# Kernel optimization log

Measured on AMD Instinct MI355X. Metric: run time of the kernel, lower is better.

The kernel has to match this reference:

```python
import jax, jax.numpy as jnp
import numpy as np

B, N, E, L, H, D = 16, 128, 2048, 4, 8, 64


def setup_inputs() -> dict:
    key = jax.random.key(0)
    k1, k2, k3, k4, k5 = jax.random.split(key, 5)
    edge_feat = jax.random.normal(k1, (B, E, D), dtype=jnp.float32)
    # index E (== num edges) is the zero-feature padding slot
    path_idx = jax.random.randint(k2, (B, N, N, L), 0, E + 1).astype(jnp.int32)
    dist = jax.random.randint(k3, (B, N, N), 0, L + 1).astype(jnp.int32)
    node_counts = jax.random.randint(k4, (B,), N // 2, N + 1).astype(jnp.int32)
    emb_table = jax.random.normal(k5, (L * H, D), dtype=jnp.float32)
    return {"edge_feat": edge_feat, "path_idx": path_idx, "dist": dist,
            "node_counts": node_counts, "emb_table": emb_table}


def reference(edge_feat, path_idx, dist, node_counts, emb_table):
    b, e, d = edge_feat.shape
    n = path_idx.shape[1]
    l = path_idx.shape[-1]
    h = emb_table.shape[0] // l
    # append zero row so padding index e gathers zeros (torch: cat zeros row)
    edata = jnp.concatenate([edge_feat, jnp.zeros((b, 1, d), edge_feat.dtype)], axis=1)
    # ragged per-graph path gather, batched: (b, n, n, l, d)
    path_data = jax.vmap(lambda ef, p: ef[p])(edata, path_idx)
    # embedding_idx = arange(h*l).reshape(l, h) -> table rows reshape to (l, h, d)
    emb = emb_table.reshape(l, h, d)
    # torch: einsum('xyld,dlh->xyh') with emb permuted (d,l,h); equivalent here
    enc = jnp.einsum('bxyld,lhd->bxyh', path_data, emb)
    dist_c = jnp.clip(dist, 1, l).astype(enc.dtype)  # clamp(min=1, max=path_len)
    enc = enc / dist_c[..., None]
    ar = jnp.arange(n)
    valid = (ar[None, :, None] < node_counts[:, None, None]) & \
            (ar[None, None, :] < node_counts[:, None, None])  # (b, n, n)
    neg_inf = jnp.asarray(-jnp.inf, enc.dtype)
    return jnp.where(valid[..., None], enc, neg_inf)
```

## Files before the change

kernel.cpp:

```cpp
#include <hip/hip_runtime.h>
#include <hip/hip_bf16.h>
#include <math.h>

#define BB 16
#define NN 128
#define EE 2048
#define LL 4
#define HH 8
#define DD 64
#define LH 32

#define NEG_SENTINEL (-1.0e30f)

typedef __attribute__((ext_vector_type(8))) short bf16x8;
typedef __attribute__((ext_vector_type(4))) float f32x4;

__device__ inline short f2bf(float f) {
    __hip_bfloat16 h = __float2bfloat16(f);
    return *(short*)&h;
}

__device__ inline bf16x8 pack_bf8(float4 a, float4 b) {
    bf16x8 r;
    r[0] = f2bf(a.x); r[1] = f2bf(a.y); r[2] = f2bf(a.z); r[3] = f2bf(a.w);
    r[4] = f2bf(b.x); r[5] = f2bf(b.y); r[6] = f2bf(b.z); r[7] = f2bf(b.w);
    return r;
}

__global__ __launch_bounds__(256) void precompute_proj_mfma(
    const float* __restrict__ edge_feat,
    const float* __restrict__ emb,
    __hip_bfloat16* __restrict__ proj)
{
    const int lane = threadIdx.x & 63;
    const int wave = threadIdx.x >> 6;
    const int tile = blockIdx.x * 4 + wave;
    const int row0 = tile * 16;
    const int m    = lane & 15;
    const int quad = lane >> 4;

    const float* arow = edge_feat + (size_t)(row0 + m) * DD + quad * 8;
    const float4 a00 = ((const float4*)arow)[0];
    const float4 a01 = ((const float4*)arow)[1];
    const float4 a10 = ((const float4*)(arow + 32))[0];
    const float4 a11 = ((const float4*)(arow + 32))[1];

    const float* br0 = emb + (size_t)m * DD + quad * 8;
    const float* br1 = emb + (size_t)(16 + m) * DD + quad * 8;
    const float4 b000 = ((const float4*)br0)[0];
    const float4 b001 = ((const float4*)br0)[1];
    const float4 b010 = ((const float4*)(br0 + 32))[0];
    const float4 b011 = ((const float4*)(br0 + 32))[1];
    const float4 b100 = ((const float4*)br1)[0];
    const float4 b101 = ((const float4*)br1)[1];
    const float4 b110 = ((const float4*)(br1 + 32))[0];
    const float4 b111 = ((const float4*)(br1 + 32))[1];

    const bf16x8 aK0  = pack_bf8(a00, a01);
    const bf16x8 aK1  = pack_bf8(a10, a11);
    const bf16x8 b0K0 = pack_bf8(b000, b001);
    const bf16x8 b0K1 = pack_bf8(b010, b011);
    const bf16x8 b1K0 = pack_bf8(b100, b101);
    const bf16x8 b1K1 = pack_bf8(b110, b111);

    f32x4 acc0 = {0.f, 0.f, 0.f, 0.f};
    f32x4 acc1 = {0.f, 0.f, 0.f, 0.f};
    acc0 = __builtin_amdgcn_mfma_f32_16x16x32_bf16(aK0, b0K0, acc0, 0, 0, 0);
    acc0 = __builtin_amdgcn_mfma_f32_16x16x32_bf16(aK1, b0K1, acc0, 0, 0, 0);
    acc1 = __builtin_amdgcn_mfma_f32_16x16x32_bf16(aK0, b1K0, acc1, 0, 0, 0);
    acc1 = __builtin_amdgcn_mfma_f32_16x16x32_bf16(aK1, b1K1, acc1, 0, 0, 0);

#pragma unroll
    for (int r = 0; r < 4; ++r) {
        const int row = row0 + quad * 4 + r;
        proj[row * LH + m]      = __float2bfloat16(acc0[r]);
        proj[row * LH + 16 + m] = __float2bfloat16(acc1[r]);
    }
}

__global__ __launch_bounds__(256) void path_gather(
    const int* __restrict__ path_idx,
    const int* __restrict__ dist,
    const int* __restrict__ node_counts,
    const __hip_bfloat16* __restrict__ proj,
    __hip_bfloat16* __restrict__ out)
{
    const int pos = blockIdx.x * blockDim.x + threadIdx.x;
    const int y   = pos & (NN - 1);
    const int x   = (pos >> 7) & (NN - 1);
    const int b   = pos >> 14;

    const int4 idx4 = ((const int4*)path_idx)[pos];
    const int  dv   = dist[pos];
    const int  nc   = node_counts[b];

    const uint4* pb = (const uint4*)(proj + (size_t)b * EE * LH);

    const int idx[4] = {idx4.x, idx4.y, idx4.z, idx4.w};
    float s[HH];
#pragma unroll
    for (int h = 0; h < HH; ++h) s[h] = 0.f;

#pragma unroll
    for (int l = 0; l < LL; ++l) {
        const int  ii    = idx[l];
        const bool live  = (ii < EE);
        uint4 v = pb[min(ii, EE - 1) * 4 + l];
        if (!live) { v.x = 0u; v.y = 0u; v.z = 0u; v.w = 0u; }
        const unsigned u[4] = {v.x, v.y, v.z, v.w};
#pragma unroll
        for (int p = 0; p < 4; ++p) {
            float flo = __uint_as_float(u[p] << 16);
            float fhi = __uint_as_float(u[p] & 0xFFFF0000u);
            s[2 * p + 0] += flo;
            s[2 * p + 1] += fhi;
        }
    }

    const int   dc = dv < 1 ? 1 : (dv > LL ? LL : dv);
    const float rd = 1.0f / (float)dc;
    const bool valid = (x < nc) && (y < nc);

    uint4 ov;
    unsigned short* po = (unsigned short*)&ov;
#pragma unroll
    for (int h = 0; h < HH; ++h) {
        const float r = valid ? s[h] * rd : NEG_SENTINEL;
        __hip_bfloat16 bh = __float2bfloat16(r);
        po[h] = *(unsigned short*)&bh;
    }
    ((uint4*)out)[pos] = ov;
}

extern "C" void kernel_launch(void* const* d_in, const int* in_sizes, int n_in,
                              void* d_out, int out_size, void* d_ws, size_t ws_size,
                              hipStream_t stream) {
    const float* edge_feat   = (const float*)d_in[0];
    const int*   path_idx    = (const int*)d_in[1];
    const int*   dist        = (const int*)d_in[2];
    const int*   node_counts = (const int*)d_in[3];
    const float* emb_table   = (const float*)d_in[4];
    __hip_bfloat16* out = (__hip_bfloat16*)d_out;

    __hip_bfloat16* proj = (__hip_bfloat16*)d_ws;

    precompute_proj_mfma<<<512, 256, 0, stream>>>(edge_feat, emb_table, proj);

    path_gather<<<1024, 256, 0, stream>>>(path_idx, dist, node_counts, proj, out);
}
```

Before: 78.04 us.

## Fuse projection and gather into one cooperative kernel with grid sync

Merges the MFMA edge-projection kernel and the path-gather kernel into one cooperative launch. A grid-wide barrier separates the two phases, so the second kernel launch and the gap between launches go away. If the cooperative launch fails, it falls back to the original two launches. The cost is the grid-sync overhead. The 1024-block grid must also stay co-resident, and half the blocks sit idle during the projection phase.

```diff
diff --git a/kernel.cpp b/kernel.cpp
--- a/kernel.cpp
+++ b/kernel.cpp
@@ -1,6 +1,9 @@
 #include <hip/hip_runtime.h>
 #include <hip/hip_bf16.h>
+#include <hip/hip_cooperative_groups.h>
 #include <math.h>
+
+namespace cg = cooperative_groups;
 
 #define BB 16
 #define NN 128
@@ -27,14 +30,12 @@
     return r;
 }
 
-__global__ __launch_bounds__(256) void precompute_proj_mfma(
+__device__ __forceinline__ void proj_tile_body(
     const float* __restrict__ edge_feat,
     const float* __restrict__ emb,
-    __hip_bfloat16* __restrict__ proj)
-{
-    const int lane = threadIdx.x & 63;
-    const int wave = threadIdx.x >> 6;
-    const int tile = blockIdx.x * 4 + wave;
+    __hip_bfloat16* __restrict__ proj,
+    int tile, int lane)
+{
     const int row0 = tile * 16;
     const int m    = lane & 15;
     const int quad = lane >> 4;
@@ -78,6 +79,93 @@
     }
 }
 
+__device__ __forceinline__ void gather_body(
+    const int* __restrict__ path_idx,
+    const int* __restrict__ dist,
+    const int* __restrict__ node_counts,
+    const __hip_bfloat16* __restrict__ proj,
+    __hip_bfloat16* __restrict__ out,
+    int pos)
+{
+    const int y = pos & (NN - 1);
+    const int x = (pos >> 7) & (NN - 1);
+    const int b = pos >> 14;
+
+    const int4 idx4 = ((const int4*)path_idx)[pos];
+    const int  dv   = dist[pos];
+    const int  nc   = node_counts[b];
+
+    const uint4* pb = (const uint4*)(proj + (size_t)b * EE * LH);
+
+    const int idx[4] = {idx4.x, idx4.y, idx4.z, idx4.w};
+    float s[HH];
+#pragma unroll
+    for (int h = 0; h < HH; ++h) s[h] = 0.f;
+
+#pragma unroll
+    for (int l = 0; l < LL; ++l) {
+        const int  ii    = idx[l];
+        const bool live  = (ii < EE);
+        uint4 v = pb[min(ii, EE - 1) * 4 + l];
+        if (!live) { v.x = 0u; v.y = 0u; v.z = 0u; v.w = 0u; }
+        const unsigned u[4] = {v.x, v.y, v.z, v.w};
+#pragma unroll
+        for (int p = 0; p < 4; ++p) {
+            float flo = __uint_as_float(u[p] << 16);
+            float fhi = __uint_as_float(u[p] & 0xFFFF0000u);
+            s[2 * p + 0] += flo;
+            s[2 * p + 1] += fhi;
+        }
+    }
+
+    const int   dc = dv < 1 ? 1 : (dv > LL ? LL : dv);
+    const float rd = 1.0f / (float)dc;
+    const bool valid = (x < nc) && (y < nc);
+
+    uint4 ov;
+    unsigned short* po = (unsigned short*)&ov;
+#pragma unroll
+    for (int h = 0; h < HH; ++h) {
+        const float r = valid ? s[h] * rd : NEG_SENTINEL;
+        __hip_bfloat16 bh = __float2bfloat16(r);
+        po[h] = *(unsigned short*)&bh;
+    }
+    ((uint4*)out)[pos] = ov;
+}
+
+__global__ __launch_bounds__(256, 4) void fused_path_encoder(
+    const float* __restrict__ edge_feat,
+    const float* __restrict__ emb,
+    const int* __restrict__ path_idx,
+    const int* __restrict__ dist,
+    const int* __restrict__ node_counts,
+    __hip_bfloat16* __restrict__ proj,
+    __hip_bfloat16* __restrict__ out)
+{
+    const int lane = threadIdx.x & 63;
+    const int wave = threadIdx.x >> 6;
+
+    if (blockIdx.x < 512) {
+        proj_tile_body(edge_feat, emb, proj, blockIdx.x * 4 + wave, lane);
+    }
+
+    __threadfence();
+    cg::this_grid().sync();
+
+    const int pos = blockIdx.x * 256 + threadIdx.x;
+    gather_body(path_idx, dist, node_counts, proj, out, pos);
+}
+
+__global__ __launch_bounds__(256) void precompute_proj_mfma(
+    const float* __restrict__ edge_feat,
+    const float* __restrict__ emb,
+    __hip_bfloat16* __restrict__ proj)
+{
+    const int lane = threadIdx.x & 63;
+    const int wave = threadIdx.x >> 6;
+    proj_tile_body(edge_feat, emb, proj, blockIdx.x * 4 + wave, lane);
+}
+
 __global__ __launch_bounds__(256) void path_gather(
     const int* __restrict__ path_idx,
     const int* __restrict__ dist,
@@ -86,50 +174,7 @@
     __hip_bfloat16* __restrict__ out)
 {
     const int pos = blockIdx.x * blockDim.x + threadIdx.x;
-    const int y   = pos & (NN - 1);
-    const int x   = (pos >> 7) & (NN - 1);
-    const int b   = pos >> 14;
-
-    const int4 idx4 = ((const int4*)path_idx)[pos];
-    const int  dv   = dist[pos];
-    const int  nc   = node_counts[b];
-
-    const uint4* pb = (const uint4*)(proj + (size_t)b * EE * LH);
-
-    const int idx[4] = {idx4.x, idx4.y, idx4.z, idx4.w};
-    float s[HH];
-#pragma unroll
-    for (int h = 0; h < HH; ++h) s[h] = 0.f;
-
-#pragma unroll
-    for (int l = 0; l < LL; ++l) {
-        const int  ii    = idx[l];
-        const bool live  = (ii < EE);
-        uint4 v = pb[min(ii, EE - 1) * 4 + l];
-        if (!live) { v.x = 0u; v.y = 0u; v.z = 0u; v.w = 0u; }
-        const unsigned u[4] = {v.x, v.y, v.z, v.w};
-#pragma unroll
-        for (int p = 0; p < 4; ++p) {
-            float flo = __uint_as_float(u[p] << 16);
-            float fhi = __uint_as_float(u[p] & 0xFFFF0000u);
-            s[2 * p + 0] += flo;
-            s[2 * p + 1] += fhi;
-        }
-    }
-
-    const int   dc = dv < 1 ? 1 : (dv > LL ? LL : dv);
-    const float rd = 1.0f / (float)dc;
-    const bool valid = (x < nc) && (y < nc);
-
-    uint4 ov;
-    unsigned short* po = (unsigned short*)&ov;
-#pragma unroll
-    for (int h = 0; h < HH; ++h) {
-        const float r = valid ? s[h] * rd : NEG_SENTINEL;
-        __hip_bfloat16 bh = __float2bfloat16(r);
-        po[h] = *(unsigned short*)&bh;
-    }
-    ((uint4*)out)[pos] = ov;
+    gather_body(path_idx, dist, node_counts, proj, out, pos);
 }
 
 extern "C" void kernel_launch(void* const* d_in, const int* in_sizes, int n_in,
@@ -144,7 +189,16 @@
 
     __hip_bfloat16* proj = (__hip_bfloat16*)d_ws;
 
-    precompute_proj_mfma<<<512, 256, 0, stream>>>(edge_feat, emb_table, proj);
-
-    path_gather<<<1024, 256, 0, stream>>>(path_idx, dist, node_counts, proj, out);
-}
+    void* kargs[] = {
+        (void*)&edge_feat, (void*)&emb_table, (void*)&path_idx,
+        (void*)&dist, (void*)&node_counts, (void*)&proj, (void*)&out
+    };
+    hipError_t e = hipLaunchCooperativeKernel(
+        reinterpret_cast<const void*>(&fused_path_encoder),
+        dim3(1024), dim3(256), kargs, 0, stream);
+
+    if (e != hipSuccess) {
+        precompute_proj_mfma<<<512, 256, 0, stream>>>(edge_feat, emb_table, proj);
+        path_gather<<<1024, 256, 0, stream>>>(path_idx, dist, node_counts, proj, out);
+    }
+}
```

Result: slower. 244.8 us (+213.7%).
